# Kernel optimization log

Measured on AMD Instinct MI355X. Metric: run time of the kernel, lower is better.

The kernel has to match this reference:

```python
import jax, jax.numpy as jnp
import numpy as np

B, S, QW, HID, HEADS = 1, 4096, 512, 512, 8
D = HID // HEADS  # size_per_head = 64
SCALE = 1.0 / np.sqrt(float(D))


def setup_inputs() -> dict:
    key = jax.random.key(0)
    k1, k2, k3, k4, k5 = jax.random.split(key, 5)
    return {
        "tensor_q": jax.random.normal(k1, (B, S, QW), dtype=jnp.float32),
        "tensor_k": jax.random.normal(k2, (B, S, QW), dtype=jnp.float32),
        "tensor_v": jax.random.normal(k3, (B, S, QW), dtype=jnp.float32),
        # in_proj_layer: [3*hidden, q_width] (torch uses rand uniform init; randn fine for reference)
        "in_proj": jax.random.normal(k4, (3 * HID, QW), dtype=jnp.float32) * 0.02,
        # out_proj: nn.Linear(hidden, out, bias=False) weight shape [out, hidden]
        "w_out": jax.random.normal(k5, (HID, HID), dtype=jnp.float32) * 0.02,
    }


def reference(tensor_q, tensor_k, tensor_v, in_proj, w_out):
    b, s, _ = tensor_q.shape
    wq, wk, wv = in_proj[:HID], in_proj[HID:2 * HID], in_proj[2 * HID:]
    # mm(W, x_2d^T)^T  ==  x_2d @ W^T ; reshape to [b, s, heads, d]
    q = (tensor_q.reshape(-1, QW) @ wq.T).reshape(b, s, HEADS, D)
    k = (tensor_k.reshape(-1, QW) @ wk.T).reshape(b, s, HEADS, D)
    v = (tensor_v.reshape(-1, QW) @ wv.T).reshape(b, s, HEADS, D)
    # scores: [b, h, s_q, s_k], explicitly materialized as in the source
    scores = jnp.einsum('bqhd,bkhd->bhqk', q, k) * SCALE
    probs = jax.nn.softmax(scores, axis=-1)
    ctx = jnp.einsum('bhqk,bkhd->bqhd', probs, v).reshape(b * s, HID)
    out = ctx @ w_out.T
    return out.reshape(b, s, HID)
```

## Files before the change

### kernel.cpp

```cpp
#include <hip/hip_runtime.h>
#include <hip/hip_bf16.h>

#define S_LEN 4096
#define QW_K  512
#define HID_N 512
#define HEADS 8
#define DH    64
#define QSCALE (0.125f * 1.4426950408889634f)

typedef _Float16 f16;
typedef _Float16 half8  __attribute__((ext_vector_type(8)));
typedef _Float16 half4v __attribute__((ext_vector_type(4)));
typedef float    float4v __attribute__((ext_vector_type(4)));
typedef float    f32x16 __attribute__((ext_vector_type(16)));
typedef unsigned int uint;
typedef unsigned int uint4v __attribute__((ext_vector_type(4)));

__device__ inline uint pkh(float a, float b) {
    return __builtin_bit_cast(uint, __builtin_amdgcn_cvt_pkrtz(a, b));
}
__device__ inline void plswap(uint& a, uint& b) {
    asm volatile("v_permlane32_swap_b32 %0, %1" : "+v"(a), "+v"(b));
}


__global__ __launch_bounds__(256) void proj_kernel(
    const float* __restrict__ xq, const float* __restrict__ xk,
    const float* __restrict__ xv, const float* __restrict__ in_proj,
    f16* __restrict__ qws, f16* __restrict__ kws, f16* __restrict__ vtws)
{
    __shared__ f16 As[128][40];
    __shared__ f16 Ws[128][40];

    const int tid  = threadIdx.x;
    const int lane = tid & 63;
    const int w    = tid >> 6;
    const int wm   = w >> 1, wn = w & 1;
    const int l15  = lane & 15, g = lane >> 4;
    const int m0   = blockIdx.x * 128;
    const int n0   = blockIdx.y * 128;
    const int matid = n0 >> 9;
    const float* A = (matid == 0) ? xq : (matid == 1) ? xk : xv;

    float4v acc[4][4];
    for (int i = 0; i < 4; i++)
        for (int j = 0; j < 4; j++)
            for (int r = 0; r < 4; r++) acc[i][j][r] = 0.0f;

    const int srow = tid >> 3;
    const int scol = (tid & 7) * 4;

    for (int k0 = 0; k0 < QW_K; k0 += 32) {
        __syncthreads();
        #pragma unroll
        for (int p = 0; p < 4; p++) {
            int r = p * 32 + srow;
            float4v av = *(const float4v*)(A + (size_t)(m0 + r) * QW_K + k0 + scol);
            float4v wv = *(const float4v*)(in_proj + (size_t)(n0 + r) * QW_K + k0 + scol);
            half4v ah, wh;
            for (int e = 0; e < 4; e++) { ah[e] = (f16)av[e]; wh[e] = (f16)wv[e]; }
            *(half4v*)&As[r][scol] = ah;
            *(half4v*)&Ws[r][scol] = wh;
        }
        __syncthreads();

        half8 a[4], b[4];
        #pragma unroll
        for (int i = 0; i < 4; i++) a[i] = *(const half8*)&As[wm * 64 + i * 16 + l15][g * 8];
        #pragma unroll
        for (int j = 0; j < 4; j++) b[j] = *(const half8*)&Ws[wn * 64 + j * 16 + l15][g * 8];
        #pragma unroll
        for (int i = 0; i < 4; i++)
            #pragma unroll
            for (int j = 0; j < 4; j++)
                acc[i][j] = __builtin_amdgcn_mfma_f32_16x16x32_f16(a[i], b[j], acc[i][j], 0, 0, 0);
    }

    #pragma unroll
    for (int i = 0; i < 4; i++) {
        int grow0 = m0 + wm * 64 + i * 16 + g * 4;
        #pragma unroll
        for (int j = 0; j < 4; j++) {
            int gcol = n0 + wn * 64 + j * 16 + l15;
            int c = gcol & 511;
            int h = c >> 6, d = c & 63;
            if (matid == 2) {
                int db = d >> 5, l31v = d & 31;
                int kb16 = grow0 >> 4;
                int g5v  = (grow0 >> 3) & 1;
                int e0   = grow0 & 7;
                half4v pv;
                for (int r = 0; r < 4; r++) pv[r] = (f16)acc[i][j][r];
                *(half4v*)(vtws + ((size_t)((h * 2 + db) * 256 + kb16) << 9)
                                + l31v * 16 + g5v * 8 + e0) = pv;
            } else if (matid == 0) {
                for (int r = 0; r < 4; r++)
                    qws[((size_t)h * S_LEN + grow0 + r) * DH + d] = (f16)(acc[i][j][r] * QSCALE);
            } else {
                int dblk = d >> 4, g5k = (d >> 3) & 1, e = d & 7;
                for (int r = 0; r < 4; r++) {
                    int s = grow0 + r;
                    kws[((size_t)((h * 128 + (s >> 5)) * 4 + dblk) << 9)
                        + (s & 31) * 16 + g5k * 8 + e] = (f16)acc[i][j][r];
                }
            }
        }
    }
}

__global__ __launch_bounds__(256) void attn_kernel(
    const f16* __restrict__ qws, const f16* __restrict__ kws,
    const f16* __restrict__ vtws, f16* __restrict__ ctxws)
{
    const int tid  = threadIdx.x;
    const int lane = tid & 63;
    const int w    = tid >> 6;
    const int l31  = lane & 31;
    const int g5   = lane >> 5;
    const int blk  = blockIdx.x;
    const int h    = blk & 7;
    const int qb   = blk >> 3;
    const int q0   = qb * 128 + w * 32;

    const f16* Kf = kws  + ((size_t)h * 128 * 4 << 9);
    const f16* Vf = vtws + ((size_t)h * 2 * 256 << 9);
    const int lo = l31 * 16 + g5 * 8;

    half8 qf[4];
    {
        const f16* qp = qws + ((size_t)h * S_LEN + q0 + l31) * DH + g5 * 8;
        #pragma unroll
        for (int dblk = 0; dblk < 4; dblk++)
            qf[dblk] = *(const half8*)(qp + dblk * 16);
    }

    float lsum = 0.0f;
    f32x16 oacc0, oacc1;
    #pragma unroll
    for (int i = 0; i < 16; i++) { oacc0[i] = 0.0f; oacc1[i] = 0.0f; }

    half8 kf[2][4];
    #pragma unroll
    for (int kb32 = 0; kb32 < 2; kb32++)
        #pragma unroll
        for (int dblk = 0; dblk < 4; dblk++)
            kf[kb32][dblk] = *(const half8*)(Kf + ((size_t)(kb32 * 4 + dblk) << 9) + lo);

    for (int t = 0; t < 64; t++) {
        const int kv0 = t * 64;

        half8 vf[2][4];
        #pragma unroll
        for (int db = 0; db < 2; db++)
            #pragma unroll
            for (int kb = 0; kb < 4; kb++)
                vf[db][kb] = *(const half8*)(Vf
                    + ((size_t)((db << 8) + (kv0 >> 4) + kb) << 9) + lo);

        f32x16 st0, st1;
        #pragma unroll
        for (int i = 0; i < 16; i++) { st0[i] = 0.0f; st1[i] = 0.0f; }
        #pragma unroll
        for (int dblk = 0; dblk < 4; dblk++) {
            st0 = __builtin_amdgcn_mfma_f32_32x32x16_f16(kf[0][dblk], qf[dblk], st0, 0, 0, 0);
            st1 = __builtin_amdgcn_mfma_f32_32x32x16_f16(kf[1][dblk], qf[dblk], st1, 0, 0, 0);
        }

        {
            const int ktn = (t < 63) ? (kv0 >> 5) + 2 : 0;
            #pragma unroll
            for (int kb32 = 0; kb32 < 2; kb32++)
                #pragma unroll
                for (int dblk = 0; dblk < 4; dblk++)
                    kf[kb32][dblk] = *(const half8*)(Kf
                        + ((size_t)((ktn + kb32) * 4 + dblk) << 9) + lo);
        }

        #pragma unroll
        for (int i = 0; i < 16; i++) {
            st0[i] = exp2f(st0[i]);
            st1[i] = exp2f(st1[i]);
        }

        f32x16 ss;
        #pragma unroll
        for (int i = 0; i < 16; i++) ss[i] = st0[i] + st1[i];
        #pragma unroll
        for (int off = 8; off >= 1; off >>= 1)
            #pragma unroll
            for (int i = 0; i < off; i++) ss[i] += ss[i + off];
        float rsum = ss[0];
        rsum += __shfl_xor(rsum, 32);
        lsum += rsum;

        half8 pf[4];
        #pragma unroll
        for (int kb = 0; kb < 2; kb++) {
            uint w0 = pkh(st0[8 * kb + 0], st0[8 * kb + 1]);
            uint w1 = pkh(st0[8 * kb + 2], st0[8 * kb + 3]);
            uint w2 = pkh(st0[8 * kb + 4], st0[8 * kb + 5]);
            uint w3 = pkh(st0[8 * kb + 6], st0[8 * kb + 7]);
            plswap(w0, w2);
            plswap(w1, w3);
            uint4v u; u[0] = w0; u[1] = w1; u[2] = w2; u[3] = w3;
            pf[kb] = __builtin_bit_cast(half8, u);
        }
        #pragma unroll
        for (int kb = 0; kb < 2; kb++) {
            uint w0 = pkh(st1[8 * kb + 0], st1[8 * kb + 1]);
            uint w1 = pkh(st1[8 * kb + 2], st1[8 * kb + 3]);
            uint w2 = pkh(st1[8 * kb + 4], st1[8 * kb + 5]);
            uint w3 = pkh(st1[8 * kb + 6], st1[8 * kb + 7]);
            plswap(w0, w2);
            plswap(w1, w3);
            uint4v u; u[0] = w0; u[1] = w1; u[2] = w2; u[3] = w3;
            pf[2 + kb] = __builtin_bit_cast(half8, u);
        }

        #pragma unroll
        for (int kb = 0; kb < 4; kb++) {
            oacc0 = __builtin_amdgcn_mfma_f32_32x32x16_f16(vf[0][kb], pf[kb], oacc0, 0, 0, 0);
            oacc1 = __builtin_amdgcn_mfma_f32_32x32x16_f16(vf[1][kb], pf[kb], oacc1, 0, 0, 0);
        }
    }

    const float inv = 1.0f / lsum;
    f16* cbase = ctxws + (size_t)(q0 + l31) * HID_N + h * DH;
    #pragma unroll
    for (int rg = 0; rg < 4; rg++) {
        half4v v0, v1;
        #pragma unroll
        for (int j = 0; j < 4; j++) {
            v0[j] = (f16)(oacc0[rg * 4 + j] * inv);
            v1[j] = (f16)(oacc1[rg * 4 + j] * inv);
        }
        const int dd = rg * 8 + g5 * 4;
        *(half4v*)(cbase + dd)      = v0;
        *(half4v*)(cbase + 32 + dd) = v1;
    }
}

__global__ __launch_bounds__(256) void outproj_kernel(
    const f16* __restrict__ ctxws, const float* __restrict__ w_out,
    float* __restrict__ out)
{
    __shared__ f16 As[128][40];
    __shared__ f16 Ws[128][40];

    const int tid  = threadIdx.x;
    const int lane = tid & 63;
    const int w    = tid >> 6;
    const int wm   = w >> 1, wn = w & 1;
    const int l15  = lane & 15, g = lane >> 4;
    const int m0   = blockIdx.x * 128;
    const int n0   = blockIdx.y * 128;

    float4v acc[4][4];
    for (int i = 0; i < 4; i++)
        for (int j = 0; j < 4; j++)
            for (int r = 0; r < 4; r++) acc[i][j][r] = 0.0f;

    const int arow = tid >> 2;
    const int acg  = (tid & 3) * 8;
    const int srow = tid >> 3;
    const int scol = (tid & 7) * 4;

    for (int k0 = 0; k0 < HID_N; k0 += 32) {
        __syncthreads();
        #pragma unroll
        for (int p = 0; p < 2; p++) {
            int r = p * 64 + arow;
            *(half8*)&As[r][acg] =
                *(const half8*)(ctxws + (size_t)(m0 + r) * HID_N + k0 + acg);
        }
        #pragma unroll
        for (int p = 0; p < 4; p++) {
            int r = p * 32 + srow;
            float4v wv = *(const float4v*)(w_out + (size_t)(n0 + r) * HID_N + k0 + scol);
            half4v wh;
            for (int e = 0; e < 4; e++) wh[e] = (f16)wv[e];
            *(half4v*)&Ws[r][scol] = wh;
        }
        __syncthreads();

        half8 a[4], b[4];
        #pragma unroll
        for (int i = 0; i < 4; i++) a[i] = *(const half8*)&As[wm * 64 + i * 16 + l15][g * 8];
        #pragma unroll
        for (int j = 0; j < 4; j++) b[j] = *(const half8*)&Ws[wn * 64 + j * 16 + l15][g * 8];
        #pragma unroll
        for (int i = 0; i < 4; i++)
            #pragma unroll
            for (int j = 0; j < 4; j++)
                acc[i][j] = __builtin_amdgcn_mfma_f32_16x16x32_f16(a[i], b[j], acc[i][j], 0, 0, 0);
    }

    #pragma unroll
    for (int i = 0; i < 4; i++) {
        int grow0 = m0 + wm * 64 + i * 16 + g * 4;
        #pragma unroll
        for (int j = 0; j < 4; j++) {
            int gcol = n0 + wn * 64 + j * 16 + l15;
            for (int r = 0; r < 4; r++)
                out[(size_t)(grow0 + r) * HID_N + gcol] = acc[i][j][r];
        }
    }
}

extern "C" void kernel_launch(void* const* d_in, const int* in_sizes, int n_in,
                              void* d_out, int out_size, void* d_ws, size_t ws_size,
                              hipStream_t stream)
{
    const float* xq      = (const float*)d_in[0];
    const float* xk      = (const float*)d_in[1];
    const float* xv      = (const float*)d_in[2];
    const float* in_proj = (const float*)d_in[3];
    const float* w_out   = (const float*)d_in[4];
    float* out = (float*)d_out;

    const size_t per = (size_t)HEADS * S_LEN * DH;
    f16* qws   = (f16*)d_ws;
    f16* kws   = qws + per;
    f16* vtws  = kws + per;
    f16* ctxws = vtws + per;

    proj_kernel<<<dim3(32, 12), 256, 0, stream>>>(xq, xk, xv, in_proj, qws, kws, vtws);
    attn_kernel<<<dim3(256), 256, 0, stream>>>(qws, kws, vtws, ctxws);
    outproj_kernel<<<dim3(32, 4), 256, 0, stream>>>(ctxws, w_out, out);
}
```

Before: 112.6 us.

## Split attention keys across waves with LDS reduction to raise block count

```diff
diff --git a/kernel.cpp b/kernel.cpp
--- a/kernel.cpp
+++ b/kernel.cpp
@@ -108,10 +108,13 @@
     }
 }
 
-__global__ __launch_bounds__(256) void attn_kernel(
+__global__ __launch_bounds__(256, 4) void attn_kernel(
     const f16* __restrict__ qws, const f16* __restrict__ kws,
     const f16* __restrict__ vtws, f16* __restrict__ ctxws)
 {
+    __shared__ float Ol[4][32][68];
+    __shared__ float Ls[4][32];
+
     const int tid  = threadIdx.x;
     const int lane = tid & 63;
     const int w    = tid >> 6;
@@ -120,7 +123,7 @@
     const int blk  = blockIdx.x;
     const int h    = blk & 7;
     const int qb   = blk >> 3;
-    const int q0   = qb * 128 + w * 32;
+    const int q0   = qb * 32;
 
     const f16* Kf = kws  + ((size_t)h * 128 * 4 << 9);
     const f16* Vf = vtws + ((size_t)h * 2 * 256 << 9);
@@ -139,15 +142,17 @@
     #pragma unroll
     for (int i = 0; i < 16; i++) { oacc0[i] = 0.0f; oacc1[i] = 0.0f; }
 
+    const int kt0 = w * 32;
+
     half8 kf[2][4];
     #pragma unroll
     for (int kb32 = 0; kb32 < 2; kb32++)
         #pragma unroll
         for (int dblk = 0; dblk < 4; dblk++)
-            kf[kb32][dblk] = *(const half8*)(Kf + ((size_t)(kb32 * 4 + dblk) << 9) + lo);
-
-    for (int t = 0; t < 64; t++) {
-        const int kv0 = t * 64;
+            kf[kb32][dblk] = *(const half8*)(Kf + ((size_t)((kt0 + kb32) * 4 + dblk) << 9) + lo);
+
+    for (int t = 0; t < 16; t++) {
+        const int kv0 = (w * 16 + t) * 64;
 
         half8 vf[2][4];
         #pragma unroll
@@ -167,7 +172,7 @@
         }
 
         {
-            const int ktn = (t < 63) ? (kv0 >> 5) + 2 : 0;
+            const int ktn = (t < 15) ? kt0 + t * 2 + 2 : kt0;
             #pragma unroll
             for (int kb32 = 0; kb32 < 2; kb32++)
                 #pragma unroll
@@ -189,9 +194,7 @@
         for (int off = 8; off >= 1; off >>= 1)
             #pragma unroll
             for (int i = 0; i < off; i++) ss[i] += ss[i + off];
-        float rsum = ss[0];
-        rsum += __shfl_xor(rsum, 32);
-        lsum += rsum;
+        lsum += ss[0];
 
         half8 pf[4];
         #pragma unroll
@@ -224,19 +227,34 @@
         }
     }
 
-    const float inv = 1.0f / lsum;
-    f16* cbase = ctxws + (size_t)(q0 + l31) * HID_N + h * DH;
+    lsum += __shfl_xor(lsum, 32);
     #pragma unroll
     for (int rg = 0; rg < 4; rg++) {
-        half4v v0, v1;
-        #pragma unroll
-        for (int j = 0; j < 4; j++) {
-            v0[j] = (f16)(oacc0[rg * 4 + j] * inv);
-            v1[j] = (f16)(oacc1[rg * 4 + j] * inv);
-        }
+        float4v v0, v1;
+        #pragma unroll
+        for (int j = 0; j < 4; j++) { v0[j] = oacc0[rg * 4 + j]; v1[j] = oacc1[rg * 4 + j]; }
         const int dd = rg * 8 + g5 * 4;
-        *(half4v*)(cbase + dd)      = v0;
-        *(half4v*)(cbase + 32 + dd) = v1;
+        *(float4v*)&Ol[w][l31][dd]      = v0;
+        *(float4v*)&Ol[w][l31][32 + dd] = v1;
+    }
+    if (g5 == 0) Ls[w][l31] = lsum;
+    __syncthreads();
+
+    #pragma unroll
+    for (int it = 0; it < 2; it++) {
+        int qd = tid * 2 + it;
+        int q  = qd >> 4;
+        int dd = (qd & 15) * 4;
+        float4v s0 = *(const float4v*)&Ol[0][q][dd];
+        float4v s1 = *(const float4v*)&Ol[1][q][dd];
+        float4v s2 = *(const float4v*)&Ol[2][q][dd];
+        float4v s3 = *(const float4v*)&Ol[3][q][dd];
+        float inv = 1.0f / (Ls[0][q] + Ls[1][q] + Ls[2][q] + Ls[3][q]);
+        half4v o;
+        #pragma unroll
+        for (int j = 0; j < 4; j++)
+            o[j] = (f16)((s0[j] + s1[j] + s2[j] + s3[j]) * inv);
+        *(half4v*)(ctxws + (size_t)(q0 + q) * HID_N + h * DH + dd) = o;
     }
 }
 
@@ -325,6 +343,6 @@
     f16* ctxws = vtws + per;
 
     proj_kernel<<<dim3(32, 12), 256, 0, stream>>>(xq, xk, xv, in_proj, qws, kws, vtws);
-    attn_kernel<<<dim3(256), 256, 0, stream>>>(qws, kws, vtws, ctxws);
+    attn_kernel<<<dim3(1024), 256, 0, stream>>>(qws, kws, vtws, ctxws);
     outproj_kernel<<<dim3(32, 4), 256, 0, stream>>>(ctxws, w_out, out);
 }
```

After: 211.5 us. +87.9%, slower.
